# Kernel optimization log

Hardware: AMD Instinct MI355X
Metric: run time of the kernel (lower is better)

The kernel has to match this reference:

```python
import jax, jax.numpy as jnp
import numpy as np

N_NODES = 50000
N_EDGES = 1_600_000
N_RELS = 8
N_BASES = 4
H_DIM = 64


def setup_inputs() -> dict:
    key = jax.random.key(0)
    ks = jax.random.split(key, 12)
    return {
        "features": jax.random.normal(ks[0], (N_NODES, 2), dtype=jnp.float32),
        "src": jax.random.randint(ks[1], (N_EDGES,), 0, N_NODES),
        "dst": jax.random.randint(ks[2], (N_EDGES,), 0, N_NODES),
        "etype": jax.random.randint(ks[3], (N_EDGES,), 0, N_RELS),
        "W_in": jax.random.normal(ks[4], (2, H_DIM), dtype=jnp.float32) * 0.5,
        "b_in": jax.random.normal(ks[5], (H_DIM,), dtype=jnp.float32) * 0.1,
        "w_comp": jax.random.normal(ks[6], (N_RELS, N_BASES), dtype=jnp.float32) * 0.5,
        "bases": jax.random.normal(ks[7], (N_BASES, H_DIM, H_DIM), dtype=jnp.float32) * (1.0 / np.sqrt(H_DIM)),
        "loop_w": jax.random.normal(ks[8], (H_DIM, H_DIM), dtype=jnp.float32) * (1.0 / np.sqrt(H_DIM)),
        "h_bias": jax.random.normal(ks[9], (H_DIM,), dtype=jnp.float32) * 0.1,
        "fc_W": jax.random.normal(ks[10], (N_NODES * H_DIM, 1), dtype=jnp.float32) * (1.0 / np.sqrt(N_NODES * H_DIM)),
        "fc_b": jax.random.normal(ks[11], (1,), dtype=jnp.float32) * 0.1,
    }


def reference(features, src, dst, etype, W_in, b_in, w_comp, bases, loop_w, h_bias, fc_W, fc_b):
    n = features.shape[0]
    # Input embedding layer: Linear(2, h_dim) on node features
    h = features @ W_in + b_in                              # [N, d]
    # Basis-decomposed relation weights: W_r = sum_b w_comp[r,b] * bases[b]
    W = jnp.einsum('rb,bio->rio', w_comp, bases)            # [R, d, d]
    # Project all nodes under each relation (low_mem grouping equivalent)
    proj = jnp.einsum('ni,rio->rno', h, W)                  # [R, N, d]
    # Gather per-edge message, scatter-add to destination (sum aggregation, norm=None)
    msg = proj[etype, src]                                  # [E, d]
    agg = jax.ops.segment_sum(msg, dst, num_segments=n)     # [N, d]
    # Self-loop + bias, activation=None, dropout omitted (eval mode)
    out = agg + h @ loop_w + h_bias                         # [N, d]
    x = out.reshape(1, -1)                                  # [1, N*d]
    return jax.nn.sigmoid(x @ fc_W + fc_b)                  # [1, 1]
```

## Files before the change

kernel.cpp:

```cpp
#include <hip/hip_runtime.h>
#include <math.h>

#define N_NODES 50000
#define N_EDGES 1600000
#define N_RELS 8
#define N_BASES 4
#define HD 64

#define NB_D 196
#define NB_E 782
#define NTHR_E (NB_E * 256)
#define NQUAD (N_EDGES / 4)

typedef int      vint4   __attribute__((ext_vector_type(4)));
typedef float    vfloat4 __attribute__((ext_vector_type(4)));
typedef _Float16 half4v  __attribute__((ext_vector_type(4)));
typedef _Float16 half8v  __attribute__((ext_vector_type(8)));

#define G_OFF      0
#define PART_OFF   1728
#define D_OFF      4096

__global__ void prep_kernel(const float* __restrict__ W_in,
                            const float* __restrict__ b_in,
                            const float* __restrict__ w_comp,
                            const float* __restrict__ bases,
                            const float* __restrict__ loop_w,
                            const float* __restrict__ h_bias,
                            float* __restrict__ G) {
    __shared__ float sA[N_BASES * 3 * HD];
    const int tid = threadIdx.x;
    const int o = tid & 63;
    const int b = tid >> 6;

    {
        float s0 = 0.f, s1 = 0.f, sb = 0.f;
        for (int i = 0; i < HD; i++) {
            float bv = bases[b * HD * HD + i * HD + o];
            s0 += W_in[i]      * bv;
            s1 += W_in[HD + i] * bv;
            sb += b_in[i]      * bv;
        }
        sA[(b * 3 + 0) * HD + o] = s0;
        sA[(b * 3 + 1) * HD + o] = s1;
        sA[(b * 3 + 2) * HD + o] = sb;
    }
    __syncthreads();

    for (int idx = tid; idx < 24 * HD; idx += 256) {
        int j = idx >> 6, oo = idx & 63;
        int r = j / 3, k = j % 3;
        float s = 0.f;
#pragma unroll
        for (int bb = 0; bb < N_BASES; bb++)
            s += w_comp[r * N_BASES + bb] * sA[(bb * 3 + k) * HD + oo];
        G[j * HD + oo] = s;
    }

    if (tid < 3 * HD) {
        int k = tid >> 6, oo = tid & 63;
        float s = 0.f;
        for (int i = 0; i < HD; i++) {
            float w = (k == 0) ? W_in[i] : (k == 1) ? W_in[HD + i] : b_in[i];
            s += w * loop_w[i * HD + oo];
        }
        if (k == 2) s += h_bias[oo];
        G[(24 + k) * HD + oo] = s;
    }
}

__global__ __launch_bounds__(256) void d_table_kernel(
        const vfloat4* __restrict__ fcW4,
        const float2* __restrict__ feat,
        const float* __restrict__ G,
        half8v* __restrict__ D16,
        float* __restrict__ partD) {
    const int v = blockIdx.x * 256 + threadIdx.x;
    float part = 0.f;

    if (v < N_NODES) {
        vfloat4 Fr[16];
#pragma unroll
        for (int k = 0; k < 16; k++) Fr[k] = __builtin_nontemporal_load(&fcW4[v * 16 + k]);

        float s[27];
#pragma unroll
        for (int j = 0; j < 27; j++) {
            float acc = 0.f;
#pragma unroll
            for (int k = 0; k < 16; k++) {
                float gx = G[j * HD + 4 * k + 0];
                float gy = G[j * HD + 4 * k + 1];
                float gz = G[j * HD + 4 * k + 2];
                float gw = G[j * HD + 4 * k + 3];
                acc += Fr[k].x * gx + Fr[k].y * gy + Fr[k].z * gz + Fr[k].w * gw;
            }
            s[j] = acc;
        }

#pragma unroll
        for (int j = 0; j < 4; j++) {
            half8v pk;
            pk[0] = (_Float16)s[6 * j + 0];
            pk[1] = (_Float16)s[6 * j + 1];
            pk[2] = (_Float16)s[6 * j + 2];
            pk[3] = (_Float16)0.f;
            pk[4] = (_Float16)s[6 * j + 3];
            pk[5] = (_Float16)s[6 * j + 4];
            pk[6] = (_Float16)s[6 * j + 5];
            pk[7] = (_Float16)0.f;
            D16[v * 4 + j] = pk;
        }

        float2 f = feat[v];
        part = s[24] * f.x + s[25] * f.y + s[26];
    }

    for (int off = 32; off; off >>= 1) part += __shfl_down(part, off);
    __shared__ float wred[4];
    if ((threadIdx.x & 63) == 0) wred[threadIdx.x >> 6] = part;
    __syncthreads();
    if (threadIdx.x == 0) partD[blockIdx.x] = wred[0] + wred[1] + wred[2] + wred[3];
}

__global__ __launch_bounds__(256) void edge_gather_kernel(
        const vint4* __restrict__ src4,
        const vint4* __restrict__ dst4,
        const vint4* __restrict__ et4,
        const float2* __restrict__ feat,
        const half4v* __restrict__ D8,
        float* __restrict__ partE) {
    const int t = blockIdx.x * 256 + threadIdx.x;
    const int t2raw = t + NTHR_E;
    const int t2 = (t2raw < NQUAD) ? t2raw : (NQUAD - 1);
    const float w2 = (t2raw < NQUAD) ? 1.f : 0.f;

    vint4 uA = __builtin_nontemporal_load(&src4[t]);
    vint4 vA = __builtin_nontemporal_load(&dst4[t]);
    vint4 rA = __builtin_nontemporal_load(&et4[t]);
    vint4 uB = __builtin_nontemporal_load(&src4[t2]);
    vint4 vB = __builtin_nontemporal_load(&dst4[t2]);
    vint4 rB = __builtin_nontemporal_load(&et4[t2]);

    float2 fA0 = feat[uA.x];
    float2 fA1 = feat[uA.y];
    float2 fA2 = feat[uA.z];
    float2 fA3 = feat[uA.w];
    float2 fB0 = feat[uB.x];
    float2 fB1 = feat[uB.y];
    float2 fB2 = feat[uB.z];
    float2 fB3 = feat[uB.w];
    half4v hA0 = D8[vA.x * 8 + rA.x];
    half4v hA1 = D8[vA.y * 8 + rA.y];
    half4v hA2 = D8[vA.z * 8 + rA.z];
    half4v hA3 = D8[vA.w * 8 + rA.w];
    half4v hB0 = D8[vB.x * 8 + rB.x];
    half4v hB1 = D8[vB.y * 8 + rB.y];
    half4v hB2 = D8[vB.z * 8 + rB.z];
    half4v hB3 = D8[vB.w * 8 + rB.w];

    float sA = fA0.x * (float)hA0.x + fA0.y * (float)hA0.y + (float)hA0.z;
    sA      += fA1.x * (float)hA1.x + fA1.y * (float)hA1.y + (float)hA1.z;
    sA      += fA2.x * (float)hA2.x + fA2.y * (float)hA2.y + (float)hA2.z;
    sA      += fA3.x * (float)hA3.x + fA3.y * (float)hA3.y + (float)hA3.z;
    float sB = fB0.x * (float)hB0.x + fB0.y * (float)hB0.y + (float)hB0.z;
    sB      += fB1.x * (float)hB1.x + fB1.y * (float)hB1.y + (float)hB1.z;
    sB      += fB2.x * (float)hB2.x + fB2.y * (float)hB2.y + (float)hB2.z;
    sB      += fB3.x * (float)hB3.x + fB3.y * (float)hB3.y + (float)hB3.z;
    float s = sA + w2 * sB;

    for (int off = 32; off; off >>= 1) s += __shfl_down(s, off);
    __shared__ float wred[4];
    if ((threadIdx.x & 63) == 0) wred[threadIdx.x >> 6] = s;
    __syncthreads();
    if (threadIdx.x == 0) partE[blockIdx.x] = wred[0] + wred[1] + wred[2] + wred[3];
}

__global__ void final_kernel(const float* __restrict__ part,
                             const float* __restrict__ fc_b,
                             float* __restrict__ out) {
    float s = 0.f;
    for (int i = threadIdx.x; i < NB_D + NB_E; i += 256) s += part[i];
    for (int off = 32; off; off >>= 1) s += __shfl_down(s, off);
    __shared__ float wred[4];
    if ((threadIdx.x & 63) == 0) wred[threadIdx.x >> 6] = s;
    __syncthreads();
    if (threadIdx.x == 0) {
        float x = wred[0] + wred[1] + wred[2] + wred[3] + fc_b[0];
        out[0] = 1.0f / (1.0f + expf(-x));
    }
}

extern "C" void kernel_launch(void* const* d_in, const int* in_sizes, int n_in,
                              void* d_out, int out_size, void* d_ws, size_t ws_size,
                              hipStream_t stream) {
    const float* features = (const float*)d_in[0];
    const int*   src      = (const int*)d_in[1];
    const int*   dst      = (const int*)d_in[2];
    const int*   etype    = (const int*)d_in[3];
    const float* W_in     = (const float*)d_in[4];
    const float* b_in     = (const float*)d_in[5];
    const float* w_comp   = (const float*)d_in[6];
    const float* bases    = (const float*)d_in[7];
    const float* loop_w   = (const float*)d_in[8];
    const float* h_bias   = (const float*)d_in[9];
    const float* fc_W     = (const float*)d_in[10];
    const float* fc_b     = (const float*)d_in[11];

    float* ws   = (float*)d_ws;
    float* G    = ws + G_OFF;
    float* part = ws + PART_OFF;
    half8v* D16 = (half8v*)(ws + D_OFF);
    half4v* D8  = (half4v*)(ws + D_OFF);
    float* out  = (float*)d_out;

    prep_kernel<<<1, 256, 0, stream>>>(W_in, b_in, w_comp, bases, loop_w, h_bias, G);
    d_table_kernel<<<NB_D, 256, 0, stream>>>(
        (const vfloat4*)fc_W, (const float2*)features, G, D16, part);
    edge_gather_kernel<<<NB_E, 256, 0, stream>>>(
        (const vint4*)src, (const vint4*)dst, (const vint4*)etype,
        (const float2*)features, D8, part + NB_D);
    final_kernel<<<1, 256, 0, stream>>>(part, fc_b, out);
}
```

Baseline: 146.4 us.

## Replace per-edge table gather with atomic scatter of source features by dst/relation

```diff
diff --git a/kernel.cpp b/kernel.cpp
--- a/kernel.cpp
+++ b/kernel.cpp
@@ -11,25 +11,32 @@
 #define NB_E 782
 #define NTHR_E (NB_E * 256)
 #define NQUAD (N_EDGES / 4)
-
-typedef int      vint4   __attribute__((ext_vector_type(4)));
-typedef float    vfloat4 __attribute__((ext_vector_type(4)));
-typedef _Float16 half4v  __attribute__((ext_vector_type(4)));
-typedef _Float16 half8v  __attribute__((ext_vector_type(8)));
-
-#define G_OFF      0
-#define PART_OFF   1728
-#define D_OFF      4096
-
-__global__ void prep_kernel(const float* __restrict__ W_in,
-                            const float* __restrict__ b_in,
-                            const float* __restrict__ w_comp,
-                            const float* __restrict__ bases,
-                            const float* __restrict__ loop_w,
-                            const float* __restrict__ h_bias,
-                            float* __restrict__ G) {
+#define NB_Z 1563
+
+typedef int   vint4   __attribute__((ext_vector_type(4)));
+typedef float vfloat4 __attribute__((ext_vector_type(4)));
+
+#define G_OFF    0
+#define PART_OFF 1728
+#define T_OFF    4096
+#define T_FLOATS (N_RELS * N_NODES * 4)
+
+__global__ __launch_bounds__(256) void zero_prep_kernel(
+        const float* __restrict__ W_in,
+        const float* __restrict__ b_in,
+        const float* __restrict__ w_comp,
+        const float* __restrict__ bases,
+        const float* __restrict__ loop_w,
+        const float* __restrict__ h_bias,
+        float* __restrict__ G,
+        vfloat4* __restrict__ T4) {
+    const int tid = threadIdx.x;
+    const int zi = blockIdx.x * 256 + tid;
+    if (zi < T_FLOATS / 4) T4[zi] = (vfloat4){0.f, 0.f, 0.f, 0.f};
+
+    if (blockIdx.x != 0) return;
+
     __shared__ float sA[N_BASES * 3 * HD];
-    const int tid = threadIdx.x;
     const int o = tid & 63;
     const int b = tid >> 6;
 
@@ -69,11 +76,57 @@
     }
 }
 
-__global__ __launch_bounds__(256) void d_table_kernel(
+__global__ __launch_bounds__(256) void edge_scatter_kernel(
+        const vint4* __restrict__ src4,
+        const vint4* __restrict__ dst4,
+        const vint4* __restrict__ et4,
+        const float2* __restrict__ feat,
+        float* __restrict__ T) {
+    const int t = blockIdx.x * 256 + threadIdx.x;
+    const int t2raw = t + NTHR_E;
+    const int t2 = (t2raw < NQUAD) ? t2raw : (NQUAD - 1);
+    const float w2 = (t2raw < NQUAD) ? 1.f : 0.f;
+
+    vint4 uA = __builtin_nontemporal_load(&src4[t]);
+    vint4 vA = __builtin_nontemporal_load(&dst4[t]);
+    vint4 rA = __builtin_nontemporal_load(&et4[t]);
+    vint4 uB = __builtin_nontemporal_load(&src4[t2]);
+    vint4 vB = __builtin_nontemporal_load(&dst4[t2]);
+    vint4 rB = __builtin_nontemporal_load(&et4[t2]);
+
+    float2 fA0 = feat[uA.x];
+    float2 fA1 = feat[uA.y];
+    float2 fA2 = feat[uA.z];
+    float2 fA3 = feat[uA.w];
+    float2 fB0 = feat[uB.x];
+    float2 fB1 = feat[uB.y];
+    float2 fB2 = feat[uB.z];
+    float2 fB3 = feat[uB.w];
+
+    int cA0 = (rA.x * N_NODES + vA.x) * 4;
+    int cA1 = (rA.y * N_NODES + vA.y) * 4;
+    int cA2 = (rA.z * N_NODES + vA.z) * 4;
+    int cA3 = (rA.w * N_NODES + vA.w) * 4;
+    int cB0 = (rB.x * N_NODES + vB.x) * 4;
+    int cB1 = (rB.y * N_NODES + vB.y) * 4;
+    int cB2 = (rB.z * N_NODES + vB.z) * 4;
+    int cB3 = (rB.w * N_NODES + vB.w) * 4;
+
+    unsafeAtomicAdd(&T[cA0 + 0], fA0.x); unsafeAtomicAdd(&T[cA0 + 1], fA0.y); unsafeAtomicAdd(&T[cA0 + 2], 1.f);
+    unsafeAtomicAdd(&T[cA1 + 0], fA1.x); unsafeAtomicAdd(&T[cA1 + 1], fA1.y); unsafeAtomicAdd(&T[cA1 + 2], 1.f);
+    unsafeAtomicAdd(&T[cA2 + 0], fA2.x); unsafeAtomicAdd(&T[cA2 + 1], fA2.y); unsafeAtomicAdd(&T[cA2 + 2], 1.f);
+    unsafeAtomicAdd(&T[cA3 + 0], fA3.x); unsafeAtomicAdd(&T[cA3 + 1], fA3.y); unsafeAtomicAdd(&T[cA3 + 2], 1.f);
+    unsafeAtomicAdd(&T[cB0 + 0], w2 * fB0.x); unsafeAtomicAdd(&T[cB0 + 1], w2 * fB0.y); unsafeAtomicAdd(&T[cB0 + 2], w2);
+    unsafeAtomicAdd(&T[cB1 + 0], w2 * fB1.x); unsafeAtomicAdd(&T[cB1 + 1], w2 * fB1.y); unsafeAtomicAdd(&T[cB1 + 2], w2);
+    unsafeAtomicAdd(&T[cB2 + 0], w2 * fB2.x); unsafeAtomicAdd(&T[cB2 + 1], w2 * fB2.y); unsafeAtomicAdd(&T[cB2 + 2], w2);
+    unsafeAtomicAdd(&T[cB3 + 0], w2 * fB3.x); unsafeAtomicAdd(&T[cB3 + 1], w2 * fB3.y); unsafeAtomicAdd(&T[cB3 + 2], w2);
+}
+
+__global__ __launch_bounds__(256) void fused_proj_kernel(
         const vfloat4* __restrict__ fcW4,
         const float2* __restrict__ feat,
         const float* __restrict__ G,
-        half8v* __restrict__ D16,
+        const vfloat4* __restrict__ T4,
         float* __restrict__ partD) {
     const int v = blockIdx.x * 256 + threadIdx.x;
     float part = 0.f;
@@ -99,21 +152,13 @@
         }
 
 #pragma unroll
-        for (int j = 0; j < 4; j++) {
-            half8v pk;
-            pk[0] = (_Float16)s[6 * j + 0];
-            pk[1] = (_Float16)s[6 * j + 1];
-            pk[2] = (_Float16)s[6 * j + 2];
-            pk[3] = (_Float16)0.f;
-            pk[4] = (_Float16)s[6 * j + 3];
-            pk[5] = (_Float16)s[6 * j + 4];
-            pk[6] = (_Float16)s[6 * j + 5];
-            pk[7] = (_Float16)0.f;
-            D16[v * 4 + j] = pk;
+        for (int r = 0; r < N_RELS; r++) {
+            vfloat4 Tc = T4[r * N_NODES + v];
+            part += Tc.x * s[3 * r] + Tc.y * s[3 * r + 1] + Tc.z * s[3 * r + 2];
         }
 
         float2 f = feat[v];
-        part = s[24] * f.x + s[25] * f.y + s[26];
+        part += s[24] * f.x + s[25] * f.y + s[26];
     }
 
     for (int off = 32; off; off >>= 1) part += __shfl_down(part, off);
@@ -123,64 +168,11 @@
     if (threadIdx.x == 0) partD[blockIdx.x] = wred[0] + wred[1] + wred[2] + wred[3];
 }
 
-__global__ __launch_bounds__(256) void edge_gather_kernel(
-        const vint4* __restrict__ src4,
-        const vint4* __restrict__ dst4,
-        const vint4* __restrict__ et4,
-        const float2* __restrict__ feat,
-        const half4v* __restrict__ D8,
-        float* __restrict__ partE) {
-    const int t = blockIdx.x * 256 + threadIdx.x;
-    const int t2raw = t + NTHR_E;
-    const int t2 = (t2raw < NQUAD) ? t2raw : (NQUAD - 1);
-    const float w2 = (t2raw < NQUAD) ? 1.f : 0.f;
-
-    vint4 uA = __builtin_nontemporal_load(&src4[t]);
-    vint4 vA = __builtin_nontemporal_load(&dst4[t]);
-    vint4 rA = __builtin_nontemporal_load(&et4[t]);
-    vint4 uB = __builtin_nontemporal_load(&src4[t2]);
-    vint4 vB = __builtin_nontemporal_load(&dst4[t2]);
-    vint4 rB = __builtin_nontemporal_load(&et4[t2]);
-
-    float2 fA0 = feat[uA.x];
-    float2 fA1 = feat[uA.y];
-    float2 fA2 = feat[uA.z];
-    float2 fA3 = feat[uA.w];
-    float2 fB0 = feat[uB.x];
-    float2 fB1 = feat[uB.y];
-    float2 fB2 = feat[uB.z];
-    float2 fB3 = feat[uB.w];
-    half4v hA0 = D8[vA.x * 8 + rA.x];
-    half4v hA1 = D8[vA.y * 8 + rA.y];
-    half4v hA2 = D8[vA.z * 8 + rA.z];
-    half4v hA3 = D8[vA.w * 8 + rA.w];
-    half4v hB0 = D8[vB.x * 8 + rB.x];
-    half4v hB1 = D8[vB.y * 8 + rB.y];
-    half4v hB2 = D8[vB.z * 8 + rB.z];
-    half4v hB3 = D8[vB.w * 8 + rB.w];
-
-    float sA = fA0.x * (float)hA0.x + fA0.y * (float)hA0.y + (float)hA0.z;
-    sA      += fA1.x * (float)hA1.x + fA1.y * (float)hA1.y + (float)hA1.z;
-    sA      += fA2.x * (float)hA2.x + fA2.y * (float)hA2.y + (float)hA2.z;
-    sA      += fA3.x * (float)hA3.x + fA3.y * (float)hA3.y + (float)hA3.z;
-    float sB = fB0.x * (float)hB0.x + fB0.y * (float)hB0.y + (float)hB0.z;
-    sB      += fB1.x * (float)hB1.x + fB1.y * (float)hB1.y + (float)hB1.z;
-    sB      += fB2.x * (float)hB2.x + fB2.y * (float)hB2.y + (float)hB2.z;
-    sB      += fB3.x * (float)hB3.x + fB3.y * (float)hB3.y + (float)hB3.z;
-    float s = sA + w2 * sB;
-
-    for (int off = 32; off; off >>= 1) s += __shfl_down(s, off);
-    __shared__ float wred[4];
-    if ((threadIdx.x & 63) == 0) wred[threadIdx.x >> 6] = s;
-    __syncthreads();
-    if (threadIdx.x == 0) partE[blockIdx.x] = wred[0] + wred[1] + wred[2] + wred[3];
-}
-
 __global__ void final_kernel(const float* __restrict__ part,
                              const float* __restrict__ fc_b,
                              float* __restrict__ out) {
     float s = 0.f;
-    for (int i = threadIdx.x; i < NB_D + NB_E; i += 256) s += part[i];
+    for (int i = threadIdx.x; i < NB_D; i += 256) s += part[i];
     for (int off = 32; off; off >>= 1) s += __shfl_down(s, off);
     __shared__ float wred[4];
     if ((threadIdx.x & 63) == 0) wred[threadIdx.x >> 6] = s;
@@ -210,15 +202,15 @@
     float* ws   = (float*)d_ws;
     float* G    = ws + G_OFF;
     float* part = ws + PART_OFF;
-    half8v* D16 = (half8v*)(ws + D_OFF);
-    half4v* D8  = (half4v*)(ws + D_OFF);
+    float* T    = ws + T_OFF;
     float* out  = (float*)d_out;
 
-    prep_kernel<<<1, 256, 0, stream>>>(W_in, b_in, w_comp, bases, loop_w, h_bias, G);
-    d_table_kernel<<<NB_D, 256, 0, stream>>>(
-        (const vfloat4*)fc_W, (const float2*)features, G, D16, part);
-    edge_gather_kernel<<<NB_E, 256, 0, stream>>>(
+    zero_prep_kernel<<<NB_Z, 256, 0, stream>>>(
+        W_in, b_in, w_comp, bases, loop_w, h_bias, G, (vfloat4*)T);
+    edge_scatter_kernel<<<NB_E, 256, 0, stream>>>(
         (const vint4*)src, (const vint4*)dst, (const vint4*)etype,
-        (const float2*)features, D8, part + NB_D);
+        (const float2*)features, T);
+    fused_proj_kernel<<<NB_D, 256, 0, stream>>>(
+        (const vfloat4*)fc_W, (const float2*)features, G, (const vfloat4*)T, part);
     final_kernel<<<1, 256, 0, stream>>>(part, fc_b, out);
 }
```

New measurement: 424.0 us. 190% more time.
